# Performance work log

Hardware: AMD Instinct MI355X
Metric: run time of the kernel (lower is better)

## Reference

```python
import jax, jax.numpy as jnp
import numpy as np

B = 8192        # batch of spots
T = 137         # target_length: number of predict heads
D = 384         # fea_size(256) + img_size(128)
K = 128         # hidden width of each head
EPS = 1e-5      # BatchNorm1d eps
SLOPE = 0.01    # LeakyReLU negative slope (torch default)


def setup_inputs() -> dict:
    key = jax.random.key(0)
    ks = jax.random.split(key, 5)
    return {
        "f":        jax.random.normal(ks[0], (B, D), dtype=jnp.float32),
        "W1":       jax.random.normal(ks[1], (T, K, D), dtype=jnp.float32) * (1.0 / np.sqrt(D)),
        "b1":       jax.random.normal(ks[2], (T, K), dtype=jnp.float32) * 0.02,
        "gamma":    jnp.ones((T, K), dtype=jnp.float32),
        "beta":     jnp.zeros((T, K), dtype=jnp.float32),
        "run_mean": jnp.zeros((T, K), dtype=jnp.float32),
        "run_var":  jnp.ones((T, K), dtype=jnp.float32),
        "W2":       jax.random.normal(ks[3], (T, K), dtype=jnp.float32) * (1.0 / np.sqrt(K)),
        "b2":       jax.random.normal(ks[4], (T,), dtype=jnp.float32) * 0.02,
    }


def reference(f, W1, b1, gamma, beta, run_mean, run_var, W2, b2):
    # Batched equivalent of: for i in range(137): Linear(384->128)+BN+LeakyReLU+Linear(128->1)
    # all applied to the same feature f; outputs concatenated -> [B, 137].
    h = jnp.einsum('bd,tkd->btk', f, W1) + b1                       # [B, T, K]
    scale = gamma * jax.lax.rsqrt(run_var + EPS)                     # eval-mode BN, [T, K]
    h = (h - run_mean) * scale + beta
    h = jnp.where(h >= 0, h, SLOPE * h)                              # LeakyReLU
    out = jnp.einsum('btk,tk->bt', h, W2) + b2                       # [B, T]
    return out
```

## Files before the change

kernel.cpp:

```cpp
#include <hip/hip_runtime.h>
#include <hip/hip_bf16.h>

constexpr int BATCH = 8192;
constexpr int THEADS = 137;
constexpr int DFEA = 384;
constexpr int KHID = 128;
constexpr float EPS_BN = 1e-5f;
constexpr float SLOPE = 0.01f;

constexpr size_t N_F  = (size_t)BATCH * DFEA;
constexpr size_t N_W1 = (size_t)THEADS * KHID * DFEA;
constexpr size_t WS_NEED = (N_F + N_W1) * sizeof(__hip_bfloat16);
constexpr int C_F8 = (int)(N_F / 8);
constexpr int C_T8 = (int)((N_F + N_W1) / 8);

typedef __attribute__((ext_vector_type(8))) short bf16x8;
typedef __attribute__((ext_vector_type(4))) float f32x4;

__device__ __forceinline__ short cvt_bf16(float x) {
    __hip_bfloat16 b = __float2bfloat16(x);
    return *(short*)&b;
}

__device__ __forceinline__ bf16x8 load8_cvt(const float* __restrict__ g) {
    f32x4 lo = *(const f32x4*)g;
    f32x4 hi = *(const f32x4*)(g + 4);
    bf16x8 r;
    r[0] = cvt_bf16(lo[0]); r[1] = cvt_bf16(lo[1]);
    r[2] = cvt_bf16(lo[2]); r[3] = cvt_bf16(lo[3]);
    r[4] = cvt_bf16(hi[0]); r[5] = cvt_bf16(hi[1]);
    r[6] = cvt_bf16(hi[2]); r[7] = cvt_bf16(hi[3]);
    return r;
}

__device__ __forceinline__ void gload16(const void* g, void* s) {
    __builtin_amdgcn_global_load_lds((const __attribute__((address_space(1))) void*)g,
                                     (__attribute__((address_space(3))) void*)s,
                                     16, 0, 0);
}

__global__ __launch_bounds__(256) void cvt_pass(const float* __restrict__ f,
                                                const float* __restrict__ W1,
                                                __hip_bfloat16* __restrict__ ws) {
    int i = blockIdx.x * 256 + threadIdx.x;
    if (i < C_F8)
        *(bf16x8*)(ws + (size_t)i * 8) = load8_cvt(f + (size_t)i * 8);
    else if (i < C_T8)
        *(bf16x8*)(ws + (size_t)i * 8) = load8_cvt(W1 + ((size_t)i - C_F8) * 8);
}

__global__ __launch_bounds__(256, 2) void fused_heads_bf16(
    const __hip_bfloat16* __restrict__ fb,
    const __hip_bfloat16* __restrict__ W1b,
    const float* __restrict__ b1,
    const float* __restrict__ gmm,
    const float* __restrict__ bta,
    const float* __restrict__ rmean,
    const float* __restrict__ rvar,
    const float* __restrict__ W2,
    const float* __restrict__ b2,
    float* __restrict__ out)
{
    __shared__ __attribute__((aligned(16))) __hip_bfloat16 As[2][256 * 32];
    __shared__ __attribute__((aligned(16))) __hip_bfloat16 Bs[2][128 * 32];

    const int tid  = threadIdx.x;
    const int lane = tid & 63;
    const int wm   = tid >> 6;
    const int m0 = blockIdx.x * 256;
    const int t  = blockIdx.y;
    const int n0 = t * KHID;

    const int row16 = lane & 15;
    const int quad  = lane >> 4;
    const int swz   = quad ^ ((row16 >> 1) & 3);

    const __hip_bfloat16* gA[4];
    const __hip_bfloat16* gB[2];
    #pragma unroll
    for (int c = 0; c < 4; ++c) {
        const int li = tid + c * 256;
        const int r = li >> 2, cb = (li & 3) ^ ((li >> 3) & 3);
        gA[c] = fb + (size_t)(m0 + r) * DFEA + cb * 8;
    }
    #pragma unroll
    for (int c = 0; c < 2; ++c) {
        const int li = tid + c * 256;
        const int r = li >> 2, cb = (li & 3) ^ ((li >> 3) & 3);
        gB[c] = W1b + (size_t)(n0 + r) * DFEA + cb * 8;
    }

    f32x4 acc[4][8];
    #pragma unroll
    for (int i = 0; i < 4; ++i)
        #pragma unroll
        for (int j = 0; j < 8; ++j)
            acc[i][j] = (f32x4){0.f, 0.f, 0.f, 0.f};

    #pragma unroll
    for (int c = 0; c < 4; ++c)
        gload16(gA[c], &As[0][(tid + c * 256) * 8]);
    #pragma unroll
    for (int c = 0; c < 2; ++c)
        gload16(gB[c], &Bs[0][(tid + c * 256) * 8]);
    __syncthreads();

    #pragma unroll 2
    for (int kt = 0; kt < DFEA / 32; ++kt) {
        const int cur = kt & 1, nxt = cur ^ 1;
        if (kt + 1 < DFEA / 32) {
            const int k1 = (kt + 1) * 32;
            #pragma unroll
            for (int c = 0; c < 4; ++c)
                gload16(gA[c] + k1, &As[nxt][(tid + c * 256) * 8]);
            #pragma unroll
            for (int c = 0; c < 2; ++c)
                gload16(gB[c] + k1, &Bs[nxt][(tid + c * 256) * 8]);
        }

        bf16x8 af[4], bfr[8];
        #pragma unroll
        for (int ai = 0; ai < 4; ++ai)
            af[ai] = *(const bf16x8*)&As[cur][(wm * 64 + ai * 16 + row16) * 32 + swz * 8];
        #pragma unroll
        for (int bi = 0; bi < 8; ++bi)
            bfr[bi] = *(const bf16x8*)&Bs[cur][(bi * 16 + row16) * 32 + swz * 8];

        #pragma unroll
        for (int ai = 0; ai < 4; ++ai)
            #pragma unroll
            for (int bi = 0; bi < 8; ++bi)
                acc[ai][bi] = __builtin_amdgcn_mfma_f32_16x16x32_bf16(
                    af[ai], bfr[bi], acc[ai][bi], 0, 0, 0);

        __syncthreads();
    }

    float s[8], cc[8], w2v[8];
    #pragma unroll
    for (int bi = 0; bi < 8; ++bi) {
        const int n = n0 + bi * 16 + row16;
        const float sv = gmm[n] * rsqrtf(rvar[n] + EPS_BN);
        s[bi]   = sv;
        cc[bi]  = bta[n] + (b1[n] - rmean[n]) * sv;
        w2v[bi] = W2[n];
    }

    float p[4][4];
    #pragma unroll
    for (int ai = 0; ai < 4; ++ai)
        #pragma unroll
        for (int r = 0; r < 4; ++r) {
            float a = 0.f;
            #pragma unroll
            for (int bi = 0; bi < 8; ++bi) {
                float y = acc[ai][bi][r] * s[bi] + cc[bi];
                y = (y >= 0.f) ? y : SLOPE * y;
                a += y * w2v[bi];
            }
            p[ai][r] = a;
        }

    #pragma unroll
    for (int mask = 1; mask <= 8; mask <<= 1)
        #pragma unroll
        for (int ai = 0; ai < 4; ++ai)
            #pragma unroll
            for (int r = 0; r < 4; ++r)
                p[ai][r] += __shfl_xor(p[ai][r], mask);

    if (row16 == 0) {
        const float bias = b2[t];
        #pragma unroll
        for (int ai = 0; ai < 4; ++ai)
            #pragma unroll
            for (int r = 0; r < 4; ++r) {
                const int row = m0 + wm * 64 + ai * 16 + quad * 4 + r;
                out[(size_t)row * THEADS + t] = p[ai][r] + bias;
            }
    }
}

__global__ __launch_bounds__(256) void fused_heads_f32(
    const float* __restrict__ f, const float* __restrict__ W1,
    const float* __restrict__ b1, const float* __restrict__ gmm,
    const float* __restrict__ bta, const float* __restrict__ rmean,
    const float* __restrict__ rvar, const float* __restrict__ W2,
    const float* __restrict__ b2, float* __restrict__ out)
{
    __shared__ __attribute__((aligned(16))) __hip_bfloat16 As[128 * 32];
    __shared__ __attribute__((aligned(16))) __hip_bfloat16 Bs[128 * 32];
    __shared__ float red[2][128];

    const int tid  = threadIdx.x;
    const int lane = tid & 63;
    const int wave = tid >> 6;
    const int wm = wave >> 1, wn = wave & 1;
    const int m0 = blockIdx.x * 128;
    const int t  = blockIdx.y;
    const int n0 = t * KHID;

    const int li0 = tid, li1 = tid + 256;
    const int r0 = li0 >> 2, c0 = (li0 & 3) * 8;
    const int r1 = li1 >> 2, c1 = (li1 & 3) * 8;
    const float* gA0 = f  + (size_t)(m0 + r0) * DFEA + c0;
    const float* gA1 = f  + (size_t)(m0 + r1) * DFEA + c1;
    const float* gB0 = W1 + (size_t)(n0 + r0) * DFEA + c0;
    const float* gB1 = W1 + (size_t)(n0 + r1) * DFEA + c1;

    const int row16 = lane & 15, quad = lane >> 4;

    f32x4 acc[4][4];
    #pragma unroll
    for (int i = 0; i < 4; ++i)
        #pragma unroll
        for (int j = 0; j < 4; ++j)
            acc[i][j] = (f32x4){0.f, 0.f, 0.f, 0.f};

    #pragma unroll 1
    for (int kt = 0; kt < DFEA / 32; ++kt) {
        const int k0 = kt * 32;
        bf16x8 va0 = load8_cvt(gA0 + k0);
        bf16x8 va1 = load8_cvt(gA1 + k0);
        bf16x8 vb0 = load8_cvt(gB0 + k0);
        bf16x8 vb1 = load8_cvt(gB1 + k0);
        __syncthreads();
        *(bf16x8*)&As[li0 * 8] = va0;
        *(bf16x8*)&As[li1 * 8] = va1;
        *(bf16x8*)&Bs[li0 * 8] = vb0;
        *(bf16x8*)&Bs[li1 * 8] = vb1;
        __syncthreads();

        bf16x8 af[4], bfr[4];
        #pragma unroll
        for (int i = 0; i < 4; ++i)
            af[i] = *(const bf16x8*)&As[(wm * 64 + i * 16 + row16) * 32 + quad * 8];
        #pragma unroll
        for (int i = 0; i < 4; ++i)
            bfr[i] = *(const bf16x8*)&Bs[(wn * 64 + i * 16 + row16) * 32 + quad * 8];
        #pragma unroll
        for (int ai = 0; ai < 4; ++ai)
            #pragma unroll
            for (int bi = 0; bi < 4; ++bi)
                acc[ai][bi] = __builtin_amdgcn_mfma_f32_16x16x32_bf16(
                    af[ai], bfr[bi], acc[ai][bi], 0, 0, 0);
    }

    float s[4], cc[4], w2v[4];
    #pragma unroll
    for (int bi = 0; bi < 4; ++bi) {
        const int n = n0 + wn * 64 + bi * 16 + row16;
        const float sv = gmm[n] * rsqrtf(rvar[n] + EPS_BN);
        s[bi] = sv;
        cc[bi] = bta[n] + (b1[n] - rmean[n]) * sv;
        w2v[bi] = W2[n];
    }
    float p[4][4];
    #pragma unroll
    for (int ai = 0; ai < 4; ++ai)
        #pragma unroll
        for (int r = 0; r < 4; ++r) {
            float a = 0.f;
            #pragma unroll
            for (int bi = 0; bi < 4; ++bi) {
                float y = acc[ai][bi][r] * s[bi] + cc[bi];
                y = (y >= 0.f) ? y : SLOPE * y;
                a += y * w2v[bi];
            }
            p[ai][r] = a;
        }
    #pragma unroll
    for (int mask = 1; mask <= 8; mask <<= 1)
        #pragma unroll
        for (int ai = 0; ai < 4; ++ai)
            #pragma unroll
            for (int r = 0; r < 4; ++r)
                p[ai][r] += __shfl_xor(p[ai][r], mask);
    if (row16 == 0) {
        #pragma unroll
        for (int ai = 0; ai < 4; ++ai)
            #pragma unroll
            for (int r = 0; r < 4; ++r)
                red[wn][wm * 64 + ai * 16 + quad * 4 + r] = p[ai][r];
    }
    __syncthreads();
    if (tid < 128)
        out[(size_t)(m0 + tid) * THEADS + t] = red[0][tid] + red[1][tid] + b2[t];
}

extern "C" void kernel_launch(void* const* d_in, const int* in_sizes, int n_in,
                              void* d_out, int out_size, void* d_ws, size_t ws_size,
                              hipStream_t stream) {
    (void)in_sizes; (void)n_in; (void)out_size;
    const float* f     = (const float*)d_in[0];
    const float* W1    = (const float*)d_in[1];
    const float* b1    = (const float*)d_in[2];
    const float* gmm   = (const float*)d_in[3];
    const float* bta   = (const float*)d_in[4];
    const float* rmean = (const float*)d_in[5];
    const float* rvar  = (const float*)d_in[6];
    const float* W2    = (const float*)d_in[7];
    const float* b2    = (const float*)d_in[8];
    float* out = (float*)d_out;

    if (ws_size >= WS_NEED) {
        __hip_bfloat16* fb  = (__hip_bfloat16*)d_ws;
        __hip_bfloat16* W1b = fb + N_F;
        cvt_pass<<<(C_T8 + 255) / 256, 256, 0, stream>>>(f, W1, fb);
        dim3 grid(BATCH / 256, THEADS);
        fused_heads_bf16<<<grid, 256, 0, stream>>>(fb, W1b, b1, gmm, bta, rmean, rvar, W2, b2, out);
    } else {
        dim3 grid(BATCH / 128, THEADS);
        fused_heads_f32<<<grid, 256, 0, stream>>>(f, W1, b1, gmm, bta, rmean, rvar, W2, b2, out);
    }
}
```

Before: 231.6 us.

## Keep full head weight tile resident in LDS with per-wave A streaming

Each 512-thread block now loads the head's entire 128x384 W1 slice into shared memory once, using an XOR swizzle. Each wave streams its own 64-row slab of the feature matrix through a private LDS buffer. Block-wide barriers in the K loop are replaced by per-wave waitcnt instructions, and the next A chunk is issued right after the fragments are read, so the load overlaps the MFMAs. This removes repeated W1 tile reloads and block synchronisation. In exchange it uses 128 KB of LDS per block, which limits occupancy to one block per CU, and A is only single-buffered per wave.

```diff
diff --git a/kernel.cpp b/kernel.cpp
--- a/kernel.cpp
+++ b/kernel.cpp
@@ -49,7 +49,7 @@
         *(bf16x8*)(ws + (size_t)i * 8) = load8_cvt(W1 + ((size_t)i - C_F8) * 8);
 }
 
-__global__ __launch_bounds__(256, 2) void fused_heads_bf16(
+__global__ __launch_bounds__(512, 2) void fused_heads_bf16(
     const __hip_bfloat16* __restrict__ fb,
     const __hip_bfloat16* __restrict__ W1b,
     const float* __restrict__ b1,
@@ -61,34 +61,49 @@
     const float* __restrict__ b2,
     float* __restrict__ out)
 {
-    __shared__ __attribute__((aligned(16))) __hip_bfloat16 As[2][256 * 32];
-    __shared__ __attribute__((aligned(16))) __hip_bfloat16 Bs[2][128 * 32];
+    __shared__ __attribute__((aligned(16))) __hip_bfloat16 smem[65536];
+    __hip_bfloat16* Bs = smem;
+    __hip_bfloat16* Aw = smem + 49152;
 
     const int tid  = threadIdx.x;
     const int lane = tid & 63;
-    const int wm   = tid >> 6;
-    const int m0 = blockIdx.x * 256;
+    const int wave = tid >> 6;
+    const int m0 = blockIdx.x * 512;
     const int t  = blockIdx.y;
     const int n0 = t * KHID;
 
     const int row16 = lane & 15;
     const int quad  = lane >> 4;
-    const int swz   = quad ^ ((row16 >> 1) & 3);
-
-    const __hip_bfloat16* gA[4];
-    const __hip_bfloat16* gB[2];
-    #pragma unroll
-    for (int c = 0; c < 4; ++c) {
-        const int li = tid + c * 256;
-        const int r = li >> 2, cb = (li & 3) ^ ((li >> 3) & 3);
-        gA[c] = fb + (size_t)(m0 + r) * DFEA + cb * 8;
-    }
-    #pragma unroll
-    for (int c = 0; c < 2; ++c) {
-        const int li = tid + c * 256;
-        const int r = li >> 2, cb = (li & 3) ^ ((li >> 3) & 3);
-        gB[c] = W1b + (size_t)(n0 + r) * DFEA + cb * 8;
-    }
+
+    #pragma unroll
+    for (int j = 0; j < 12; ++j) {
+        const int li = tid + j * 512;
+        const int r  = li / 48, cp = li % 48;
+        const int c  = (cp & ~7) | ((cp ^ r) & 7);
+        gload16(W1b + (size_t)(n0 + r) * DFEA + c * 8, &Bs[(size_t)li * 8]);
+    }
+
+    const __hip_bfloat16* aSrc[4];
+    #pragma unroll
+    for (int j = 0; j < 4; ++j) {
+        const int r = j * 16 + (lane >> 2);
+        const int c = (lane & 3) ^ ((lane >> 3) & 3);
+        aSrc[j] = fb + (size_t)(m0 + wave * 64 + r) * DFEA + c * 8;
+    }
+    __hip_bfloat16* aDst = Aw + wave * 2048;
+
+    #pragma unroll
+    for (int j = 0; j < 4; ++j)
+        gload16(aSrc[j], aDst + j * 512 + lane * 8);
+
+    __syncthreads();
+
+    const int aoff = wave * 2048 + row16 * 32 + (quad ^ ((row16 >> 1) & 3)) * 8;
+    const int u0 = quad ^ (row16 & 7);
+    int bbase[8];
+    #pragma unroll
+    for (int bi = 0; bi < 8; ++bi)
+        bbase[bi] = (bi * 16 + row16) * DFEA;
 
     f32x4 acc[4][8];
     #pragma unroll
@@ -98,33 +113,27 @@
             acc[i][j] = (f32x4){0.f, 0.f, 0.f, 0.f};
 
     #pragma unroll
-    for (int c = 0; c < 4; ++c)
-        gload16(gA[c], &As[0][(tid + c * 256) * 8]);
-    #pragma unroll
-    for (int c = 0; c < 2; ++c)
-        gload16(gB[c], &Bs[0][(tid + c * 256) * 8]);
-    __syncthreads();
-
-    #pragma unroll 2
     for (int kt = 0; kt < DFEA / 32; ++kt) {
-        const int cur = kt & 1, nxt = cur ^ 1;
+        __builtin_amdgcn_s_waitcnt(0x0F70);
+
+        bf16x8 af[4], bfr[8];
+        #pragma unroll
+        for (int ai = 0; ai < 4; ++ai)
+            af[ai] = *(const bf16x8*)&Aw[aoff - wave * 2048 + wave * 2048 + ai * 512];
+        const int gcb = (4 * kt) & ~7;
+        const int v   = u0 ^ ((kt & 1) << 2);
+        #pragma unroll
+        for (int bi = 0; bi < 8; ++bi)
+            bfr[bi] = *(const bf16x8*)&Bs[bbase[bi] + (gcb + v) * 8];
+
+        __builtin_amdgcn_s_waitcnt(0xC07F);
+
         if (kt + 1 < DFEA / 32) {
             const int k1 = (kt + 1) * 32;
             #pragma unroll
-            for (int c = 0; c < 4; ++c)
-                gload16(gA[c] + k1, &As[nxt][(tid + c * 256) * 8]);
-            #pragma unroll
-            for (int c = 0; c < 2; ++c)
-                gload16(gB[c] + k1, &Bs[nxt][(tid + c * 256) * 8]);
+            for (int j = 0; j < 4; ++j)
+                gload16(aSrc[j] + k1, aDst + j * 512 + lane * 8);
         }
-
-        bf16x8 af[4], bfr[8];
-        #pragma unroll
-        for (int ai = 0; ai < 4; ++ai)
-            af[ai] = *(const bf16x8*)&As[cur][(wm * 64 + ai * 16 + row16) * 32 + swz * 8];
-        #pragma unroll
-        for (int bi = 0; bi < 8; ++bi)
-            bfr[bi] = *(const bf16x8*)&Bs[cur][(bi * 16 + row16) * 32 + swz * 8];
 
         #pragma unroll
         for (int ai = 0; ai < 4; ++ai)
@@ -132,8 +141,6 @@
             for (int bi = 0; bi < 8; ++bi)
                 acc[ai][bi] = __builtin_amdgcn_mfma_f32_16x16x32_bf16(
                     af[ai], bfr[bi], acc[ai][bi], 0, 0, 0);
-
-        __syncthreads();
     }
 
     float s[8], cc[8], w2v[8];
@@ -175,7 +182,7 @@
         for (int ai = 0; ai < 4; ++ai)
             #pragma unroll
             for (int r = 0; r < 4; ++r) {
-                const int row = m0 + wm * 64 + ai * 16 + quad * 4 + r;
+                const int row = m0 + wave * 64 + ai * 16 + quad * 4 + r;
                 out[(size_t)row * THEADS + t] = p[ai][r] + bias;
             }
     }
@@ -307,8 +314,8 @@
         __hip_bfloat16* fb  = (__hip_bfloat16*)d_ws;
         __hip_bfloat16* W1b = fb + N_F;
         cvt_pass<<<(C_T8 + 255) / 256, 256, 0, stream>>>(f, W1, fb);
-        dim3 grid(BATCH / 256, THEADS);
-        fused_heads_bf16<<<grid, 256, 0, stream>>>(fb, W1b, b1, gmm, bta, rmean, rvar, W2, b2, out);
+        dim3 grid(BATCH / 512, THEADS);
+        fused_heads_bf16<<<grid, 512, 0, stream>>>(fb, W1b, b1, gmm, bta, rmean, rvar, W2, b2, out);
     } else {
         dim3 grid(BATCH / 128, THEADS);
         fused_heads_f32<<<grid, 256, 0, stream>>>(f, W1, b1, gmm, bta, rmean, rvar, W2, b2, out);
```

After: 223.9 us. 3.3% less time.
